# Kernel optimization log

Hardware: AMD Instinct MI355X
Metric: run time of the kernel (lower is better)

## Reference

```python
import jax, jax.numpy as jnp
import numpy as np

D_MODEL = 1024
HEAD = 16
K_D = D_MODEL // HEAD
SEQ_LEN = 2048
BATCH = 4
NEG = 1e10


def setup_inputs() -> dict:
    key = jax.random.key(0)
    ks = jax.random.split(key, 5)
    x = jax.random.normal(ks[0], (BATCH, SEQ_LEN, D_MODEL), dtype=jnp.float32)
    # params (torch Linear stored as [out,in]; we store [in,out] and matmul directly)
    W_attn = jax.random.normal(ks[1], (D_MODEL, 3 * D_MODEL), dtype=jnp.float32) * 0.02
    b_attn = jnp.zeros((3 * D_MODEL,), dtype=jnp.float32)
    W_proj = jax.random.normal(ks[2], (D_MODEL, D_MODEL), dtype=jnp.float32) * 0.02
    b_proj = jnp.zeros((D_MODEL,), dtype=jnp.float32)
    return {"x": x, "W_attn": W_attn, "b_attn": b_attn, "W_proj": W_proj, "b_proj": b_proj}


def reference(x, W_attn, b_attn, W_proj, b_proj):
    B, S, D = x.shape
    qkv = x @ W_attn + b_attn                     # [B,S,3D]
    # NOTE: source splits as (value, query, key) in that order
    value, query, key = jnp.split(qkv, 3, axis=-1)

    def heads(t):  # [B,S,D] -> [B,H,S,k_d]
        return t.reshape(B, S, HEAD, K_D).transpose(0, 2, 1, 3)

    v, q, k = heads(value), heads(query), heads(key)
    present = jnp.stack((k, v))                   # [2,B,H,S,k_d]

    scores = jnp.einsum('bhqd,bhkd->bhqk', q, k) / jnp.sqrt(jnp.float32(K_D))
    bias = jnp.tril(jnp.ones((S, S), dtype=scores.dtype))[None, None]
    scores = scores * bias - NEG * (1.0 - bias)
    attn = jax.nn.softmax(scores, axis=-1)
    out = jnp.einsum('bhqk,bhkd->bhqd', attn, v)  # [B,H,S,k_d]
    out = out.transpose(0, 2, 1, 3).reshape(B, S, D)
    out = out @ W_proj + b_proj
    return out, present
```

## Files before the change

### kernel.cpp

```cpp
#include <hip/hip_runtime.h>

typedef __attribute__((ext_vector_type(8))) short short8;
typedef __attribute__((ext_vector_type(4))) short short4v;
typedef __attribute__((ext_vector_type(4))) float f32x4;
typedef __attribute__((ext_vector_type(16))) float f32x16;
typedef __attribute__((ext_vector_type(4))) unsigned int u32x4;
typedef unsigned int u32;

#define D_MODEL 1024
#define HEADS 16
#define KD 64
#define SEQ 2048
#define BATCH 4
#define NTOK (BATCH*SEQ)
#define QKV_N (3*D_MODEL)

__device__ inline float bf2f(unsigned short u) {
    unsigned x = ((unsigned)u) << 16;
    return __builtin_bit_cast(float, x);
}
__device__ inline unsigned short f2bf(float f) {
    unsigned u = __builtin_bit_cast(unsigned, f);
    u += 0x7FFFu + ((u >> 16) & 1u);
    return (unsigned short)(u >> 16);
}
__device__ __forceinline__ void gload_lds16(const unsigned short* g, unsigned short* l) {
    __builtin_amdgcn_global_load_lds(
        (const __attribute__((address_space(1))) void*)g,
        (__attribute__((address_space(3))) void*)l, 16, 0, 0);
}
__device__ __forceinline__ u32 cvtpk(float lo, float hi) {
    u32 r; asm("v_cvt_pk_bf16_f32 %0, %1, %2" : "=v"(r) : "v"(lo), "v"(hi)); return r;
}

__global__ __launch_bounds__(256) void cvt_kernel(
    const float* __restrict__ x, unsigned short* __restrict__ y)
{
    size_t i = (size_t)blockIdx.x * 256 + threadIdx.x;
    f32x4 a = *reinterpret_cast<const f32x4*>(x + i*8);
    f32x4 b = *reinterpret_cast<const f32x4*>(x + i*8 + 4);
    short8 o;
    #pragma unroll
    for (int j = 0; j < 4; ++j) { o[j] = (short)f2bf(a[j]); o[j+4] = (short)f2bf(b[j]); }
    *reinterpret_cast<short8*>(y + i*8) = o;
}

__global__ __launch_bounds__(256) void transpose_kernel(
    const float* __restrict__ W, unsigned short* __restrict__ WT, int K, int N)
{
    __shared__ unsigned short T[64][80];
    const int tid = threadIdx.x;
    const int n0 = blockIdx.x * 64, k0 = blockIdx.y * 64;

    int r  = tid >> 2;
    int cq = tid & 3;
    const float* src = W + (size_t)(k0 + r) * N + n0 + cq*16;
    #pragma unroll
    for (int q = 0; q < 4; ++q) {
        f32x4 v = *reinterpret_cast<const f32x4*>(src + q*4);
        #pragma unroll
        for (int j = 0; j < 4; ++j) T[cq*16 + q*4 + j][r] = f2bf(v[j]);
    }
    __syncthreads();
    int c  = tid >> 2;
    int rq = tid & 3;
    short8 o0 = *reinterpret_cast<const short8*>(&T[c][rq*16]);
    short8 o1 = *reinterpret_cast<const short8*>(&T[c][rq*16 + 8]);
    unsigned short* dst = WT + (size_t)(n0 + c) * K + k0 + rq*16;
    *reinterpret_cast<short8*>(dst)     = o0;
    *reinterpret_cast<short8*>(dst + 8) = o1;
}

template<int Y_F32, int VTG>
__global__ __launch_bounds__(256) void gemm_bt_kernel(
    const unsigned short* __restrict__ A, const unsigned short* __restrict__ BT,
    const float* __restrict__ bias, void* __restrict__ Yv,
    unsigned short* __restrict__ vtg,
    int M, int N, int K)
{
    __shared__ unsigned short sA[128*64];
    __shared__ unsigned short sB[128*64];

    const int tid = threadIdx.x, lane = tid & 63, w = tid >> 6;
    const int l15 = lane & 15, lg = lane >> 4;

    const int nwg = gridDim.x * gridDim.y;
    const int bid = blockIdx.y * gridDim.x + blockIdx.x;
    const int swz = (bid & 7) * (nwg >> 3) + (bid >> 3);
    const int n0 = (swz % gridDim.x) * 128;
    const int m0 = (swz / gridDim.x) * 128;

    const int wr = w >> 1, wc = w & 1;

    f32x4 acc[4][4];
    #pragma unroll
    for (int m = 0; m < 4; ++m)
        #pragma unroll
        for (int n = 0; n < 4; ++n) acc[m][n] = f32x4{0,0,0,0};

    const int ldrow = (lane >> 3);
    const int slot  = lane & 7;

    for (int k0 = 0; k0 < K; k0 += 64) {
        #pragma unroll
        for (int i = 0; i < 4; ++i) {
            int kb  = w*4 + i;
            int row = kb*8 + ldrow;
            int sc  = slot ^ (row & 7);
            gload_lds16(&A [(size_t)(m0 + row) * K + k0 + sc*8], &sA[kb*512]);
            gload_lds16(&BT[(size_t)(n0 + row) * K + k0 + sc*8], &sB[kb*512]);
        }
        __syncthreads();

        #pragma unroll
        for (int kk = 0; kk < 2; ++kk) {
            short8 af[4], bfr[4];
            #pragma unroll
            for (int m = 0; m < 4; ++m) {
                int row = wr*64 + m*16 + l15;
                int ch  = (4*kk + lg) ^ (row & 7);
                af[m] = *reinterpret_cast<const short8*>(&sA[row*64 + ch*8]);
            }
            #pragma unroll
            for (int n = 0; n < 4; ++n) {
                int row = wc*64 + n*16 + l15;
                int ch  = (4*kk + lg) ^ (row & 7);
                bfr[n] = *reinterpret_cast<const short8*>(&sB[row*64 + ch*8]);
            }
            __builtin_amdgcn_s_setprio(1);
            #pragma unroll
            for (int m = 0; m < 4; ++m)
                #pragma unroll
                for (int n = 0; n < 4; ++n)
                    acc[m][n] = __builtin_amdgcn_mfma_f32_16x16x32_bf16(
                        af[m], bfr[n], acc[m][n], 0, 0, 0);
            __builtin_amdgcn_s_setprio(0);
        }
        __syncthreads();
    }

    #pragma unroll
    for (int n = 0; n < 4; ++n) {
        int col = n0 + wc*64 + n*16 + l15;
        float bv = bias[col];
        #pragma unroll
        for (int m = 0; m < 4; ++m) {
            int row0 = m0 + wr*64 + m*16 + lg*4;
            float v0 = acc[m][n][0] + bv;
            float v1 = acc[m][n][1] + bv;
            float v2 = acc[m][n][2] + bv;
            float v3 = acc[m][n][3] + bv;
            if (Y_F32) {
                float* Y = (float*)Yv;
                Y[(size_t)(row0+0) * N + col] = v0;
                Y[(size_t)(row0+1) * N + col] = v1;
                Y[(size_t)(row0+2) * N + col] = v2;
                Y[(size_t)(row0+3) * N + col] = v3;
            } else {
                unsigned short* Y = (unsigned short*)Yv;
                Y[(size_t)(row0+0) * N + col] = f2bf(v0);
                Y[(size_t)(row0+1) * N + col] = f2bf(v1);
                Y[(size_t)(row0+2) * N + col] = f2bf(v2);
                Y[(size_t)(row0+3) * N + col] = f2bf(v3);
            }
            if (VTG && n0 < D_MODEL) {
                int hh = col >> 6, dd = col & 63;
                int bb = row0 >> 11, ss = row0 & (SEQ - 1);
                short4v pk;
                pk[0] = (short)f2bf(v0); pk[1] = (short)f2bf(v1);
                pk[2] = (short)f2bf(v2); pk[3] = (short)f2bf(v3);
                *reinterpret_cast<short4v*>(
                    vtg + (((size_t)bb*HEADS + hh)*KD + dd)*SEQ + ss) = pk;
            }
        }
    }
}

__global__ __launch_bounds__(256) void present_kernel(
    const unsigned short* __restrict__ qkv, float* __restrict__ pres)
{
    int i  = blockIdx.x * 256 + threadIdx.x;
    int d8 = i & 7;
    int s  = (i >> 3)  & (SEQ - 1);
    int h  = (i >> 14) & (HEADS - 1);
    int bb = (i >> 18) & 3;
    int kv = i >> 20;
    int col = (kv == 0 ? 2*D_MODEL : 0) + h*KD + d8*8;
    short8 v = *reinterpret_cast<const short8*>(
        qkv + (size_t)(bb*SEQ + s) * QKV_N + col);
    f32x4 lo, hi;
    #pragma unroll
    for (int j = 0; j < 4; ++j) {
        lo[j] = bf2f((unsigned short)v[j]);
        hi[j] = bf2f((unsigned short)v[j + 4]);
    }
    *reinterpret_cast<f32x4*>(pres + (size_t)i * 8)     = lo;
    *reinterpret_cast<f32x4*>(pres + (size_t)i * 8 + 4) = hi;
}

__global__ __launch_bounds__(256) void attn_kernel(
    const unsigned short* __restrict__ qkv,
    const unsigned short* __restrict__ vtg,
    unsigned short* __restrict__ aout)
{
    __shared__ unsigned short Kl[2][64*64];
    __shared__ unsigned short Vl[2][64*64];

    const int tid  = threadIdx.x;
    const int lane = tid & 63;
    const int w    = tid >> 6;
    const int l31  = lane & 31, hi = lane >> 5;

    const int qpair = blockIdx.x;
    const int h  = blockIdx.y;
    const int b  = blockIdx.z;

    const unsigned short* base  = qkv + (size_t)b * SEQ * QKV_N;
    const unsigned short* vbase = vtg + ((size_t)b * HEADS + h) * KD * SEQ;
    const int qoff = D_MODEL + h*KD;
    const int koff = 2*D_MODEL + h*KD;

    const float SCALE2 = 0.125f * 1.44269504088896f;
    const float THR_RAW = 44.36f;

    const int ldrow = lane >> 3;
    const int slot  = lane & 7;

    for (int pass = 0; pass < 2; ++pass) {
        const int qb = pass ? (15 - qpair) : qpair;
        const int q0 = qb * 128;
        const int qrow  = q0 + w*32 + l31;
        const int qminw = q0 + w*32;

        short8 qf[4];
        #pragma unroll
        for (int ks = 0; ks < 4; ++ks)
            qf[ks] = *reinterpret_cast<const short8*>(
                base + (size_t)qrow * QKV_N + qoff + ks*16 + hi*8);

        f32x16 o0, o1;
        #pragma unroll
        for (int r = 0; r < 16; ++r) { o0[r] = 0.f; o1[r] = 0.f; }
        float m = -1e30f, msc = -1e30f * 0.180336887f, sr = 0.f;

        const int nt = q0/64 + 2;

        #pragma unroll
        for (int i = 0; i < 2; ++i) {
            int kb = w*2 + i, row = kb*8 + ldrow, sc = slot ^ (row & 7);
            gload_lds16(&base[(size_t)row * QKV_N + koff + sc*8], &Kl[0][kb*512]);
            gload_lds16(&vbase[(size_t)row * SEQ + sc*8],         &Vl[0][kb*512]);
        }
        __syncthreads();

        for (int t = 0; t < nt; ++t) {
            const int buf = t & 1;

            if (t + 1 < nt) {
                #pragma unroll
                for (int i = 0; i < 2; ++i) {
                    int kb = w*2 + i, row = kb*8 + ldrow, sc = slot ^ (row & 7);
                    gload_lds16(&base[(size_t)((t+1)*64 + row) * QKV_N + koff + sc*8],
                                &Kl[buf^1][kb*512]);
                    gload_lds16(&vbase[(size_t)row * SEQ + (t+1)*64 + sc*8],
                                &Vl[buf^1][kb*512]);
                }
            }

            #pragma unroll
            for (int h32 = 0; h32 < 2; ++h32) {
                const int kb0 = t*64 + h32*32;
                if (kb0 < qminw + 32) {
                    f32x16 s;
                    #pragma unroll
                    for (int r = 0; r < 16; ++r) s[r] = 0.f;
                    const int krow = h32*32 + l31;
                    const int ksw  = krow & 7;
                    __builtin_amdgcn_s_setprio(1);
                    #pragma unroll
                    for (int ks = 0; ks < 4; ++ks) {
                        short8 kf = *reinterpret_cast<const short8*>(
                            &Kl[buf][krow*64 + ((2*ks + hi) ^ ksw)*8]);
                        s = __builtin_amdgcn_mfma_f32_32x32x16_bf16(kf, qf[ks], s, 0, 0, 0);
                    }
                    __builtin_amdgcn_s_setprio(0);

                    if (kb0 == qminw) {
                        const int kq = l31 - 4*hi;
                        #pragma unroll
                        for (int r = 0; r < 16; ++r) {
                            const int cr = (r & 3) + 8*(r >> 2);
                            s[r] = (cr <= kq) ? s[r] : -1e30f;
                        }
                    }

                    float pm = s[0];
                    #pragma unroll
                    for (int r = 1; r < 16; ++r) pm = fmaxf(pm, s[r]);
                    pm = fmaxf(pm, __shfl_xor(pm, 32, 64));
                    if (!__all(pm <= m + THR_RAW)) {
                        float mn  = fmaxf(m, pm);
                        float fac = exp2f((m - mn) * SCALE2);
                        sr *= fac;
                        #pragma unroll
                        for (int r = 0; r < 16; ++r) { o0[r] *= fac; o1[r] *= fac; }
                        m = mn; msc = m * SCALE2;
                    }

                    float ts = 0.f;
                    #pragma unroll
                    for (int r = 0; r < 16; ++r) {
                        float pv = exp2f(s[r]*SCALE2 - msc);
                        s[r] = pv;
                        ts += pv;
                    }
                    sr += ts + __shfl_xor(ts, 32, 64);

                    u32 W[8];
                    #pragma unroll
                    for (int wi = 0; wi < 8; ++wi) W[wi] = cvtpk(s[2*wi], s[2*wi+1]);

                    #pragma unroll
                    for (int ks = 0; ks < 2; ++ks) {
                        u32 s0 = hi ? W[4*ks+0] : W[4*ks+2];
                        u32 s1 = hi ? W[4*ks+1] : W[4*ks+3];
                        u32 r0 = (u32)__shfl_xor((int)s0, 32, 64);
                        u32 r1 = (u32)__shfl_xor((int)s1, 32, 64);
                        u32x4 wv;
                        wv[0] = hi ? r0 : W[4*ks+0];
                        wv[1] = hi ? r1 : W[4*ks+1];
                        wv[2] = hi ? W[4*ks+2] : r0;
                        wv[3] = hi ? W[4*ks+3] : r1;
                        short8 pfrag = __builtin_bit_cast(short8, wv);
                        __builtin_amdgcn_s_setprio(1);
                        #pragma unroll
                        for (int dt = 0; dt < 2; ++dt) {
                            const int vrow = dt*32 + l31;
                            const int vch  = (4*h32 + 2*ks + hi) ^ (vrow & 7);
                            short8 vf = *reinterpret_cast<const short8*>(
                                &Vl[buf][vrow*64 + vch*8]);
                            if (dt == 0)
                                o0 = __builtin_amdgcn_mfma_f32_32x32x16_bf16(vf, pfrag, o0, 0, 0, 0);
                            else
                                o1 = __builtin_amdgcn_mfma_f32_32x32x16_bf16(vf, pfrag, o1, 0, 0, 0);
                        }
                        __builtin_amdgcn_s_setprio(0);
                    }
                }
            }
            __syncthreads();
        }

        const float inv = 1.0f / sr;
        unsigned short* orow = aout + ((size_t)b * SEQ + qrow) * D_MODEL + h*KD;
        #pragma unroll
        for (int dt = 0; dt < 2; ++dt) {
            #pragma unroll
            for (int g = 0; g < 4; ++g) {
                short4v pk;
                #pragma unroll
                for (int j = 0; j < 4; ++j) {
                    float v = (dt == 0 ? o0[4*g + j] : o1[4*g + j]) * inv;
                    pk[j] = (short)f2bf(v);
                }
                *reinterpret_cast<short4v*>(orow + dt*32 + 8*g + 4*hi) = pk;
            }
        }
    }
}

extern "C" void kernel_launch(void* const* d_in, const int* in_sizes, int n_in,
                              void* d_out, int out_size, void* d_ws, size_t ws_size,
                              hipStream_t stream)
{
    const float* x      = (const float*)d_in[0];
    const float* W_attn = (const float*)d_in[1];
    const float* b_attn = (const float*)d_in[2];
    const float* W_proj = (const float*)d_in[3];
    const float* b_proj = (const float*)d_in[4];
    float* out = (float*)d_out;

    unsigned short* qkv  = (unsigned short*)d_ws;
    unsigned short* xbf  = qkv + (size_t)NTOK * QKV_N;
    unsigned short* aout = xbf;
    unsigned short* WT   = xbf + (size_t)NTOK * D_MODEL;
    unsigned short* WpT  = WT + (size_t)QKV_N * D_MODEL;
    unsigned short* vtg  = WpT + (size_t)D_MODEL * D_MODEL;

    cvt_kernel<<<(NTOK * D_MODEL / 8) / 256, 256, 0, stream>>>(x, xbf);
    dim3 gt1(QKV_N / 64, D_MODEL / 64);
    transpose_kernel<<<gt1, 256, 0, stream>>>(W_attn, WT, D_MODEL, QKV_N);
    dim3 gt2(D_MODEL / 64, D_MODEL / 64);
    transpose_kernel<<<gt2, 256, 0, stream>>>(W_proj, WpT, D_MODEL, D_MODEL);

    dim3 g1(QKV_N / 128, NTOK / 128);
    gemm_bt_kernel<0, 1><<<g1, 256, 0, stream>>>(xbf, WT, b_attn, qkv, vtg,
                                                 NTOK, QKV_N, D_MODEL);

    present_kernel<<<(2 * BATCH * HEADS * SEQ * 8) / 256, 256, 0, stream>>>(
        qkv, out + (size_t)NTOK * D_MODEL);

    dim3 ga(SEQ / 256, HEADS, BATCH);
    attn_kernel<<<ga, 256, 0, stream>>>(qkv, vtg, aout);

    dim3 g2(D_MODEL / 128, NTOK / 128);
    gemm_bt_kernel<1, 0><<<g2, 256, 0, stream>>>(aout, WpT, b_proj, out, nullptr,
                                                 NTOK, D_MODEL, D_MODEL);
}
```

Measured before the change: 219.2 us.

## Fuse present writes into QKV GEMM and restructure attention inner loop

Removes the separate present kernel by having the QKV GEMM epilogue write K and V directly as fp32 into the present output, using the unrounded fp32 values. The attention kernel now processes both 32-key halves of each 64-key tile together, doing one shared max/rescale and sum per tile instead of per half. It uses permlane32_swap for the cross-half reductions and flattens the grid to 1D so heads and batches are interleaved across workgroups. The trade-off is heavier strided scalar fp32 stores in the GEMM epilogue and more live registers in attention.

```diff
diff --git a/kernel.cpp b/kernel.cpp
--- a/kernel.cpp
+++ b/kernel.cpp
@@ -5,6 +5,7 @@
 typedef __attribute__((ext_vector_type(4))) float f32x4;
 typedef __attribute__((ext_vector_type(16))) float f32x16;
 typedef __attribute__((ext_vector_type(4))) unsigned int u32x4;
+typedef __attribute__((ext_vector_type(2))) unsigned int u32x2;
 typedef unsigned int u32;
 
 #define D_MODEL 1024
@@ -31,6 +32,29 @@
 }
 __device__ __forceinline__ u32 cvtpk(float lo, float hi) {
     u32 r; asm("v_cvt_pk_bf16_f32 %0, %1, %2" : "=v"(r) : "v"(lo), "v"(hi)); return r;
+}
+__device__ __forceinline__ void pl32swap(u32& a, u32& b) {
+#if __has_builtin(__builtin_amdgcn_permlane32_swap)
+    u32x2 r = __builtin_amdgcn_permlane32_swap(a, b, 0, 0);
+    a = r[0]; b = r[1];
+#else
+    u32 pa = (u32)__shfl_xor((int)a, 32, 64);
+    u32 pb = (u32)__shfl_xor((int)b, 32, 64);
+    bool hb = (threadIdx.x & 32) != 0;
+    u32 na = hb ? pb : a;
+    u32 nb = hb ? b : pa;
+    a = na; b = nb;
+#endif
+}
+__device__ __forceinline__ float pairmax(float x) {
+    u32 a = __builtin_bit_cast(u32, x), b = a;
+    pl32swap(a, b);
+    return fmaxf(x, fmaxf(__builtin_bit_cast(float, a), __builtin_bit_cast(float, b)));
+}
+__device__ __forceinline__ float pairsum(float x) {
+    u32 a = __builtin_bit_cast(u32, x), b = a;
+    pl32swap(a, b);
+    return __builtin_bit_cast(float, a) + __builtin_bit_cast(float, b);
 }
 
 __global__ __launch_bounds__(256) void cvt_kernel(
@@ -71,11 +95,11 @@
     *reinterpret_cast<short8*>(dst + 8) = o1;
 }
 
-template<int Y_F32, int VTG>
+template<int Y_F32, int FUSE>
 __global__ __launch_bounds__(256) void gemm_bt_kernel(
     const unsigned short* __restrict__ A, const unsigned short* __restrict__ BT,
     const float* __restrict__ bias, void* __restrict__ Yv,
-    unsigned short* __restrict__ vtg,
+    unsigned short* __restrict__ vtg, float* __restrict__ pres,
     int M, int N, int K)
 {
     __shared__ unsigned short sA[128*64];
@@ -163,7 +187,7 @@
                 Y[(size_t)(row0+2) * N + col] = f2bf(v2);
                 Y[(size_t)(row0+3) * N + col] = f2bf(v3);
             }
-            if (VTG && n0 < D_MODEL) {
+            if (FUSE && n0 < D_MODEL) {
                 int hh = col >> 6, dd = col & 63;
                 int bb = row0 >> 11, ss = row0 & (SEQ - 1);
                 short4v pk;
@@ -171,31 +195,19 @@
                 pk[2] = (short)f2bf(v2); pk[3] = (short)f2bf(v3);
                 *reinterpret_cast<short4v*>(
                     vtg + (((size_t)bb*HEADS + hh)*KD + dd)*SEQ + ss) = pk;
+                float* pv = pres + (size_t)BATCH*HEADS*SEQ*KD
+                          + (((size_t)bb*HEADS + hh)*SEQ + ss)*KD + dd;
+                pv[0] = v0; pv[KD] = v1; pv[2*KD] = v2; pv[3*KD] = v3;
+            }
+            if (FUSE && n0 >= 2*D_MODEL) {
+                int rel = col - 2*D_MODEL;
+                int hh = rel >> 6, dd = rel & 63;
+                int bb = row0 >> 11, ss = row0 & (SEQ - 1);
+                float* pk2 = pres + (((size_t)bb*HEADS + hh)*SEQ + ss)*KD + dd;
+                pk2[0] = v0; pk2[KD] = v1; pk2[2*KD] = v2; pk2[3*KD] = v3;
             }
         }
     }
-}
-
-__global__ __launch_bounds__(256) void present_kernel(
-    const unsigned short* __restrict__ qkv, float* __restrict__ pres)
-{
-    int i  = blockIdx.x * 256 + threadIdx.x;
-    int d8 = i & 7;
-    int s  = (i >> 3)  & (SEQ - 1);
-    int h  = (i >> 14) & (HEADS - 1);
-    int bb = (i >> 18) & 3;
-    int kv = i >> 20;
-    int col = (kv == 0 ? 2*D_MODEL : 0) + h*KD + d8*8;
-    short8 v = *reinterpret_cast<const short8*>(
-        qkv + (size_t)(bb*SEQ + s) * QKV_N + col);
-    f32x4 lo, hi;
-    #pragma unroll
-    for (int j = 0; j < 4; ++j) {
-        lo[j] = bf2f((unsigned short)v[j]);
-        hi[j] = bf2f((unsigned short)v[j + 4]);
-    }
-    *reinterpret_cast<f32x4*>(pres + (size_t)i * 8)     = lo;
-    *reinterpret_cast<f32x4*>(pres + (size_t)i * 8 + 4) = hi;
 }
 
 __global__ __launch_bounds__(256) void attn_kernel(
@@ -211,9 +223,10 @@
     const int w    = tid >> 6;
     const int l31  = lane & 31, hi = lane >> 5;
 
-    const int qpair = blockIdx.x;
-    const int h  = blockIdx.y;
-    const int b  = blockIdx.z;
+    const int bid   = blockIdx.x;
+    const int hb    = bid & 63;
+    const int qpair = bid >> 6;
+    const int h = hb & 15, b = hb >> 4;
 
     const unsigned short* base  = qkv + (size_t)b * SEQ * QKV_N;
     const unsigned short* vbase = vtg + ((size_t)b * HEADS + h) * KD * SEQ;
@@ -225,6 +238,7 @@
 
     const int ldrow = lane >> 3;
     const int slot  = lane & 7;
+    const int ksw   = l31 & 7;
 
     for (int pass = 0; pass < 2; ++pass) {
         const int qb = pass ? (15 - qpair) : qpair;
@@ -243,7 +257,7 @@
         for (int r = 0; r < 16; ++r) { o0[r] = 0.f; o1[r] = 0.f; }
         float m = -1e30f, msc = -1e30f * 0.180336887f, sr = 0.f;
 
-        const int nt = q0/64 + 2;
+        const int nt = 2*qb + 2;
 
         #pragma unroll
         for (int i = 0; i < 2; ++i) {
@@ -267,78 +281,95 @@
                 }
             }
 
-            #pragma unroll
-            for (int h32 = 0; h32 < 2; ++h32) {
-                const int kb0 = t*64 + h32*32;
-                if (kb0 < qminw + 32) {
-                    f32x16 s;
-                    #pragma unroll
-                    for (int r = 0; r < 16; ++r) s[r] = 0.f;
-                    const int krow = h32*32 + l31;
-                    const int ksw  = krow & 7;
-                    __builtin_amdgcn_s_setprio(1);
-                    #pragma unroll
-                    for (int ks = 0; ks < 4; ++ks) {
-                        short8 kf = *reinterpret_cast<const short8*>(
-                            &Kl[buf][krow*64 + ((2*ks + hi) ^ ksw)*8]);
-                        s = __builtin_amdgcn_mfma_f32_32x32x16_bf16(kf, qf[ks], s, 0, 0, 0);
-                    }
-                    __builtin_amdgcn_s_setprio(0);
-
-                    if (kb0 == qminw) {
-                        const int kq = l31 - 4*hi;
-                        #pragma unroll
-                        for (int r = 0; r < 16; ++r) {
-                            const int cr = (r & 3) + 8*(r >> 2);
-                            s[r] = (cr <= kq) ? s[r] : -1e30f;
-                        }
-                    }
-
-                    float pm = s[0];
-                    #pragma unroll
-                    for (int r = 1; r < 16; ++r) pm = fmaxf(pm, s[r]);
-                    pm = fmaxf(pm, __shfl_xor(pm, 32, 64));
-                    if (!__all(pm <= m + THR_RAW)) {
-                        float mn  = fmaxf(m, pm);
-                        float fac = exp2f((m - mn) * SCALE2);
-                        sr *= fac;
-                        #pragma unroll
-                        for (int r = 0; r < 16; ++r) { o0[r] *= fac; o1[r] *= fac; }
-                        m = mn; msc = m * SCALE2;
-                    }
-
-                    float ts = 0.f;
+            const int d0 = qminw - t*64;
+            if (d0 > -32) {
+                f32x16 sa, sb;
+                #pragma unroll
+                for (int r = 0; r < 16; ++r) { sa[r] = 0.f; sb[r] = 0.f; }
+                __builtin_amdgcn_s_setprio(1);
+                #pragma unroll
+                for (int ks = 0; ks < 4; ++ks) {
+                    short8 kf = *reinterpret_cast<const short8*>(
+                        &Kl[buf][l31*64 + ((2*ks + hi) ^ ksw)*8]);
+                    sa = __builtin_amdgcn_mfma_f32_32x32x16_bf16(kf, qf[ks], sa, 0, 0, 0);
+                }
+                #pragma unroll
+                for (int ks = 0; ks < 4; ++ks) {
+                    short8 kf = *reinterpret_cast<const short8*>(
+                        &Kl[buf][(32 + l31)*64 + ((2*ks + hi) ^ ksw)*8]);
+                    sb = __builtin_amdgcn_mfma_f32_32x32x16_bf16(kf, qf[ks], sb, 0, 0, 0);
+                }
+                __builtin_amdgcn_s_setprio(0);
+
+                if (d0 <= 32) {
+                    const int kqA = l31 + d0      - 4*hi;
+                    const int kqB = l31 + d0 - 32 - 4*hi;
                     #pragma unroll
                     for (int r = 0; r < 16; ++r) {
-                        float pv = exp2f(s[r]*SCALE2 - msc);
-                        s[r] = pv;
-                        ts += pv;
+                        const int cr = (r & 3) + 8*(r >> 2);
+                        if (d0 == 0) sa[r] = (cr <= kqA) ? sa[r] : -1e30f;
+                        sb[r] = (cr <= kqB) ? sb[r] : -1e30f;
                     }
-                    sr += ts + __shfl_xor(ts, 32, 64);
-
-                    u32 W[8];
+                }
+
+                float x[8];
+                #pragma unroll
+                for (int i = 0; i < 8; ++i)
+                    x[i] = fmaxf(fmaxf(sa[2*i], sa[2*i+1]), fmaxf(sb[2*i], sb[2*i+1]));
+                float pm = fmaxf(fmaxf(fmaxf(x[0], x[1]), fmaxf(x[2], x[3])),
+                                 fmaxf(fmaxf(x[4], x[5]), fmaxf(x[6], x[7])));
+                pm = pairmax(pm);
+                if (!__all(pm <= m + THR_RAW)) {
+                    float mn  = fmaxf(m, pm);
+                    float fac = exp2f((m - mn) * SCALE2);
+                    sr *= fac;
                     #pragma unroll
-                    for (int wi = 0; wi < 8; ++wi) W[wi] = cvtpk(s[2*wi], s[2*wi+1]);
-
+                    for (int r = 0; r < 16; ++r) { o0[r] *= fac; o1[r] *= fac; }
+                    m = mn; msc = m * SCALE2;
+                }
+
+                #pragma unroll
+                for (int r = 0; r < 16; ++r) {
+                    sa[r] = exp2f(sa[r]*SCALE2 - msc);
+                    sb[r] = exp2f(sb[r]*SCALE2 - msc);
+                }
+                float u[8];
+                #pragma unroll
+                for (int i = 0; i < 8; ++i)
+                    u[i] = (sa[2*i] + sa[2*i+1]) + (sb[2*i] + sb[2*i+1]);
+                float ts = ((u[0]+u[1]) + (u[2]+u[3])) + ((u[4]+u[5]) + (u[6]+u[7]));
+                sr += pairsum(ts);
+
+                u32 WA[8], WB[8];
+                #pragma unroll
+                for (int wi = 0; wi < 8; ++wi) {
+                    WA[wi] = cvtpk(sa[2*wi], sa[2*wi+1]);
+                    WB[wi] = cvtpk(sb[2*wi], sb[2*wi+1]);
+                }
+
+                #pragma unroll
+                for (int h32 = 0; h32 < 2; ++h32) {
                     #pragma unroll
                     for (int ks = 0; ks < 2; ++ks) {
-                        u32 s0 = hi ? W[4*ks+0] : W[4*ks+2];
-                        u32 s1 = hi ? W[4*ks+1] : W[4*ks+3];
+                        u32 W0 = h32 ? WB[4*ks+0] : WA[4*ks+0];
+                        u32 W1 = h32 ? WB[4*ks+1] : WA[4*ks+1];
+                        u32 W2 = h32 ? WB[4*ks+2] : WA[4*ks+2];
+                        u32 W3 = h32 ? WB[4*ks+3] : WA[4*ks+3];
+                        u32 s0 = hi ? W0 : W2;
+                        u32 s1 = hi ? W1 : W3;
                         u32 r0 = (u32)__shfl_xor((int)s0, 32, 64);
                         u32 r1 = (u32)__shfl_xor((int)s1, 32, 64);
                         u32x4 wv;
-                        wv[0] = hi ? r0 : W[4*ks+0];
-                        wv[1] = hi ? r1 : W[4*ks+1];
-                        wv[2] = hi ? W[4*ks+2] : r0;
-                        wv[3] = hi ? W[4*ks+3] : r1;
+                        wv[0] = hi ? r0 : W0;
+                        wv[1] = hi ? r1 : W1;
+                        wv[2] = hi ? W2 : r0;
+                        wv[3] = hi ? W3 : r1;
                         short8 pfrag = __builtin_bit_cast(short8, wv);
                         __builtin_amdgcn_s_setprio(1);
                         #pragma unroll
                         for (int dt = 0; dt < 2; ++dt) {
-                            const int vrow = dt*32 + l31;
-                            const int vch  = (4*h32 + 2*ks + hi) ^ (vrow & 7);
                             short8 vf = *reinterpret_cast<const short8*>(
-                                &Vl[buf][vrow*64 + vch*8]);
+                                &Vl[buf][(dt*32 + l31)*64 + ((4*h32 + 2*ks + hi) ^ ksw)*8]);
                             if (dt == 0)
                                 o0 = __builtin_amdgcn_mfma_f32_32x32x16_bf16(vf, pfrag, o0, 0, 0, 0);
                             else
@@ -386,6 +417,7 @@
     unsigned short* WT   = xbf + (size_t)NTOK * D_MODEL;
     unsigned short* WpT  = WT + (size_t)QKV_N * D_MODEL;
     unsigned short* vtg  = WpT + (size_t)D_MODEL * D_MODEL;
+    float* pres = out + (size_t)NTOK * D_MODEL;
 
     cvt_kernel<<<(NTOK * D_MODEL / 8) / 256, 256, 0, stream>>>(x, xbf);
     dim3 gt1(QKV_N / 64, D_MODEL / 64);
@@ -394,16 +426,13 @@
     transpose_kernel<<<gt2, 256, 0, stream>>>(W_proj, WpT, D_MODEL, D_MODEL);
 
     dim3 g1(QKV_N / 128, NTOK / 128);
-    gemm_bt_kernel<0, 1><<<g1, 256, 0, stream>>>(xbf, WT, b_attn, qkv, vtg,
+    gemm_bt_kernel<0, 1><<<g1, 256, 0, stream>>>(xbf, WT, b_attn, qkv, vtg, pres,
                                                  NTOK, QKV_N, D_MODEL);
 
-    present_kernel<<<(2 * BATCH * HEADS * SEQ * 8) / 256, 256, 0, stream>>>(
-        qkv, out + (size_t)NTOK * D_MODEL);
-
-    dim3 ga(SEQ / 256, HEADS, BATCH);
-    attn_kernel<<<ga, 256, 0, stream>>>(qkv, vtg, aout);
+    attn_kernel<<<512, 256, 0, stream>>>(qkv, vtg, aout);
 
     dim3 g2(D_MODEL / 128, NTOK / 128);
-    gemm_bt_kernel<1, 0><<<g2, 256, 0, stream>>>(aout, WpT, b_proj, out, nullptr,
+    gemm_bt_kernel<1, 0><<<g2, 256, 0, stream>>>(aout, WpT, b_proj, out,
+                                                 nullptr, nullptr,
                                                  NTOK, D_MODEL, D_MODEL);
 }
```

Measured after the change: 216.7 us. No clear change (-1.1%).
